# Optimization experiments

Hardware: AMD Instinct MI355X
Metric: run time of the kernel (lower is better)

The kernel has to match this reference:

```python
import jax, jax.numpy as jnp
import numpy as np

TOK_DIM, POS_DIM, HEAD_DIM = 3, 3, 64
D_MODEL, T, B = 128, 4096, 8


def setup_inputs() -> dict:
    key = jax.random.key(0)
    ks = jax.random.split(key, 8)
    s = 0.1
    return {
        "x": jax.random.normal(ks[0], (B, T, TOK_DIM + POS_DIM), jnp.float32),
        "Wq1": jax.random.normal(ks[1], (TOK_DIM, HEAD_DIM), jnp.float32) * s,
        "Wk1": jax.random.normal(ks[2], (TOK_DIM, HEAD_DIM), jnp.float32) * s,
        "Wv1": jax.random.normal(ks[3], (TOK_DIM, HEAD_DIM), jnp.float32) * s,
        "Wq2": jax.random.normal(ks[4], (POS_DIM, HEAD_DIM), jnp.float32) * s,
        "Wk2": jax.random.normal(ks[5], (POS_DIM, HEAD_DIM), jnp.float32) * s,
        "Wv2": jax.random.normal(ks[6], (POS_DIM, HEAD_DIM), jnp.float32) * s,
        "Wout": jax.random.normal(ks[7], (2 * HEAD_DIM, D_MODEL), jnp.float32) * s,
    }


def _attend(q, k, v):
    # q,k,v: [B,T,HEAD_DIM]; causal scaled dot-product attention
    scale = 1.0 / np.sqrt(HEAD_DIM).astype(np.float32)
    scores = jnp.einsum('btd,bsd->bts', q, k) * scale  # [B,T,T]
    t = scores.shape[1]
    causal = jnp.arange(t)[:, None] >= jnp.arange(t)[None, :]
    scores = jnp.where(causal[None], scores, -jnp.inf)
    p = jax.nn.softmax(scores, axis=-1)
    return jnp.einsum('bts,bsd->btd', p, v)


def reference(x, Wq1, Wk1, Wv1, Wq2, Wk2, Wv2, Wout):
    x_tok = x[:, :, :TOK_DIM]
    x_pos = x[:, :, TOK_DIM:]
    out1 = _attend(x_tok @ Wq1, x_tok @ Wk1, x_tok @ Wv1)
    out2 = _attend(x_pos @ Wq2, x_pos @ Wk2, x_pos @ Wv2)
    out = jnp.concatenate([out1, out2], axis=-1)  # [B,T,2*HEAD_DIM]
    return out @ Wout  # [B,T,D_MODEL]
```

## Files before the change

### kernel.cpp

```cpp
#include <hip/hip_runtime.h>
#include <hip/hip_bf16.h>
#include <stdint.h>

#define T_SEQ 4096

typedef float  f32x4   __attribute__((ext_vector_type(4)));
typedef float  f32x16  __attribute__((ext_vector_type(16)));
typedef short  bf16x8  __attribute__((ext_vector_type(8)));
typedef unsigned int u32x2 __attribute__((ext_vector_type(2)));
typedef unsigned int u32x4 __attribute__((ext_vector_type(4)));

typedef const __attribute__((address_space(1))) uint32_t* gptr_t;
typedef __attribute__((address_space(3))) uint32_t* lptr_t;

__device__ __forceinline__ uint32_t f2bf1(float f) {
    uint32_t u = __float_as_uint(f);
    return (u + 0x7fffu + ((u >> 16) & 1u)) >> 16;
}
__device__ __forceinline__ short f2bfs(float f) { return (short)f2bf1(f); }
__device__ __forceinline__ uint32_t cvtpk(float lo, float hi) {
    uint32_t r;
    asm("v_cvt_pk_bf16_f32 %0, %1, %2" : "=v"(r) : "v"(lo), "v"(hi));
    return r;
}

__global__ __launch_bounds__(256) void qk_proj(
    const float* __restrict__ x,
    const float* __restrict__ Wq1, const float* __restrict__ Wk1,
    const float* __restrict__ Wq2, const float* __restrict__ Wk2,
    short* __restrict__ Q, short* __restrict__ K)
{
    int idx = blockIdx.x * 256 + threadIdx.x;
    int d = idx & 63;
    int t = (idx >> 6) & (T_SEQ - 1);
    int b = idx >> 18;
    const float* xp = x + (size_t)(b * T_SEQ + t) * 6;
    float x0 = xp[0], x1 = xp[1], x2 = xp[2];
    float x3 = xp[3], x4 = xp[4], x5 = xp[5];
    const float QS = 0.125f * 1.44269504088896340736f;
    float q1 = (x0 * Wq1[d] + x1 * Wq1[64 + d] + x2 * Wq1[128 + d]) * QS;
    float k1 =  x0 * Wk1[d] + x1 * Wk1[64 + d] + x2 * Wk1[128 + d];
    float q2 = (x3 * Wq2[d] + x4 * Wq2[64 + d] + x5 * Wq2[128 + d]) * QS;
    float k2 =  x3 * Wk2[d] + x4 * Wk2[64 + d] + x5 * Wk2[128 + d];
    size_t base1 = ((size_t)(b * 2 + 0) * T_SEQ + t) * 64 + d;
    size_t base2 = ((size_t)(b * 2 + 1) * T_SEQ + t) * 64 + d;
    Q[base1] = f2bfs(q1);  Q[base2] = f2bfs(q2);
    K[base1] = f2bfs(k1);  K[base2] = f2bfs(k2);
}

__global__ __launch_bounds__(256) void v_proj_t(
    const float* __restrict__ x,
    const float* __restrict__ Wv1, const float* __restrict__ Wv2,
    short* __restrict__ Vt)
{
    int bh = blockIdx.x >> 6;
    int tt = blockIdx.x & 63;
    int head = bh & 1, b = bh >> 1;
    int t  = tt * 64 + (threadIdx.x & 63);
    int dg = threadIdx.x >> 6;
    const float* Wv = head ? Wv2 : Wv1;
    const float* xp = x + (size_t)(b * T_SEQ + t) * 6 + head * 3;
    float x0 = xp[0], x1 = xp[1], x2 = xp[2];
    size_t base = (size_t)bh * 64 * T_SEQ + t;
    #pragma unroll
    for (int k = 0; k < 16; ++k) {
        int d = dg * 16 + k;
        float v = x0 * Wv[d] + x1 * Wv[64 + d] + x2 * Wv[128 + d];
        Vt[base + (size_t)d * T_SEQ] = f2bfs(v);
    }
}

__global__ __launch_bounds__(128, 2) void attn(
    const short* __restrict__ Q, const short* __restrict__ K,
    const short* __restrict__ Vt, float* __restrict__ Hf)
{
    __shared__ __align__(16) char smem[32768];

    int id = blockIdx.x;
    int xcd = id & 7, j = id >> 3;
    int bh = xcd * 2 + (j & 1);
    int i  = j >> 1;
    int tid = threadIdx.x;
    int W = tid >> 6;
    int lane = tid & 63;
    int ql = lane & 31, h = lane >> 5;
    int t0A = 32 * i, t0B = 32 * (127 - i);
    int qA = t0A + ql, qB = t0B + ql;
    int sweep = ((127 - i) >> 1) + 1;

    size_t kvbase = (size_t)bh * (T_SEQ * 64);

    bf16x8 qfA[4], qfB[4];
    #pragma unroll
    for (int ks = 0; ks < 4; ++ks) {
        qfA[ks] = *(const bf16x8*)(Q + kvbase + (size_t)qA * 64 + ks * 16 + h * 8);
        qfB[ks] = *(const bf16x8*)(Q + kvbase + (size_t)qB * 64 + ks * 16 + h * 8);
    }

    int row16 = tid >> 3;
    int scol = ((tid & 7) ^ (row16 & 7)) * 8;
    const short* ksrc = K  + kvbase + (size_t)row16 * 64 + scol;
    const short* vsrc = Vt + kvbase + (size_t)row16 * T_SEQ + scol;

    f32x16 accA0, accA1, accB0, accB1;
    #pragma unroll
    for (int r = 0; r < 16; ++r) { accA0[r]=0.f; accA1[r]=0.f; accB0[r]=0.f; accB1[r]=0.f; }
    float lA = 0.f, lB = 0.f;

#define STAGE(nb, kvv)                                                          \
    _Pragma("unroll")                                                           \
    for (int z = 0; z < 4; ++z) {                                               \
        __builtin_amdgcn_global_load_lds(                                       \
            (gptr_t)(ksrc + (size_t)((kvv) + z * 16) * 64),                     \
            (lptr_t)((nb) + z * 2048 + W * 1024), 16, 0, 0);                    \
        __builtin_amdgcn_global_load_lds(                                       \
            (gptr_t)(vsrc + (size_t)(z * 16) * T_SEQ + (kvv)),                  \
            (lptr_t)((nb) + 8192 + z * 2048 + W * 1024), 16, 0, 0);             \
    }

    STAGE(smem, 0);
    __syncthreads();

    int swz = (ql & 7) << 4;

    for (int c = 0; c < sweep; ++c) {
        const int kv0 = c * 64;
        if (c + 1 < sweep) { char* nb = smem + ((c + 1) & 1) * 16384; STAGE(nb, kv0 + 64); }
        const char* ldsK = smem + (c & 1) * 16384;
        const char* ldsV = ldsK + 8192;

        bool actA = (kv0 + 32 * W <= t0A + 31);
        bool actB = (kv0 + 32 * W <= t0B + 31);

        const char* krow = ldsK + (32 * W + ql) * 128;
        bf16x8 kf0 = *(const bf16x8*)(krow + ((0 * 32 + h * 16) ^ swz));
        bf16x8 kf1 = *(const bf16x8*)(krow + ((1 * 32 + h * 16) ^ swz));
        bf16x8 kf2 = *(const bf16x8*)(krow + ((2 * 32 + h * 16) ^ swz));
        bf16x8 kf3 = *(const bf16x8*)(krow + ((3 * 32 + h * 16) ^ swz));

        bf16x8 pfA0, pfA1, pfB0, pfB1;

#define QK_SM(Sv, qfX, qX, lX, pf0, pf1)                                        \
        {                                                                       \
            f32x16 Sv;                                                          \
            _Pragma("unroll") for (int r = 0; r < 16; ++r) Sv[r] = 0.f;         \
            Sv = __builtin_amdgcn_mfma_f32_32x32x16_bf16(kf0, qfX[0], Sv,0,0,0);\
            Sv = __builtin_amdgcn_mfma_f32_32x32x16_bf16(kf1, qfX[1], Sv,0,0,0);\
            Sv = __builtin_amdgcn_mfma_f32_32x32x16_bf16(kf2, qfX[2], Sv,0,0,0);\
            Sv = __builtin_amdgcn_mfma_f32_32x32x16_bf16(kf3, qfX[3], Sv,0,0,0);\
            bool needmask = (kv0 + 32 * W + 31 > qX - ql);    \
            float pp[16];                                                       \
            _Pragma("unroll") for (int r = 0; r < 16; ++r) {                    \
                float pv = __builtin_amdgcn_exp2f(Sv[r]);                       \
                if (needmask) {                                                 \
                    int kv = kv0 + 32 * W + (r & 3) + 8 * (r >> 2) + 4 * h;     \
                    pv = (kv <= qX) ? pv : 0.f;                                 \
                }                                                               \
                pp[r] = pv;                                                     \
            }                                                                   \
            lX += (((pp[0]+pp[1])+(pp[2]+pp[3])) + ((pp[4]+pp[5])+(pp[6]+pp[7])))\
                + (((pp[8]+pp[9])+(pp[10]+pp[11])) + ((pp[12]+pp[13])+(pp[14]+pp[15])));\
            uint32_t pw[8];                                                     \
            _Pragma("unroll") for (int e = 0; e < 8; ++e)                       \
                pw[e] = cvtpk(pp[2*e], pp[2*e+1]);                              \
            {                                                                   \
                uint32_t a0 = pw[0], b0 = pw[2], a1 = pw[1], b1 = pw[3];        \
                asm("v_permlane32_swap_b32 %0, %1" : "+v"(a0), "+v"(b0));       \
                asm("v_permlane32_swap_b32 %0, %1" : "+v"(a1), "+v"(b1));       \
                u32x4 fr = {a0, a1, b0, b1};                                    \
                pf0 = __builtin_bit_cast(bf16x8, fr);                           \
                uint32_t c0 = pw[4], d0 = pw[6], c1 = pw[5], d1 = pw[7];        \
                asm("v_permlane32_swap_b32 %0, %1" : "+v"(c0), "+v"(d0));       \
                asm("v_permlane32_swap_b32 %0, %1" : "+v"(c1), "+v"(d1));       \
                u32x4 fr1 = {c0, c1, d0, d1};                                   \
                pf1 = __builtin_bit_cast(bf16x8, fr1);                          \
            }                                                                   \
        }

        if (actB) QK_SM(SB, qfB, qB, lB, pfB0, pfB1)
        if (actA) QK_SM(SA, qfA, qA, lA, pfA0, pfA1)

        int cb0 = (2 * W + 0) * 32 + h * 16;
        int cb1 = (2 * W + 1) * 32 + h * 16;
        bf16x8 vf00 = *(const bf16x8*)(ldsV + ql * 128        + (cb0 ^ swz));
        bf16x8 vf01 = *(const bf16x8*)(ldsV + ql * 128        + (cb1 ^ swz));
        bf16x8 vf10 = *(const bf16x8*)(ldsV + (32 + ql) * 128 + (cb0 ^ swz));
        bf16x8 vf11 = *(const bf16x8*)(ldsV + (32 + ql) * 128 + (cb1 ^ swz));

        if (actB) {
            accB0 = __builtin_amdgcn_mfma_f32_32x32x16_bf16(vf00, pfB0, accB0, 0, 0, 0);
            accB0 = __builtin_amdgcn_mfma_f32_32x32x16_bf16(vf01, pfB1, accB0, 0, 0, 0);
            accB1 = __builtin_amdgcn_mfma_f32_32x32x16_bf16(vf10, pfB0, accB1, 0, 0, 0);
            accB1 = __builtin_amdgcn_mfma_f32_32x32x16_bf16(vf11, pfB1, accB1, 0, 0, 0);
        }
        if (actA) {
            accA0 = __builtin_amdgcn_mfma_f32_32x32x16_bf16(vf00, pfA0, accA0, 0, 0, 0);
            accA0 = __builtin_amdgcn_mfma_f32_32x32x16_bf16(vf01, pfA1, accA0, 0, 0, 0);
            accA1 = __builtin_amdgcn_mfma_f32_32x32x16_bf16(vf10, pfA0, accA1, 0, 0, 0);
            accA1 = __builtin_amdgcn_mfma_f32_32x32x16_bf16(vf11, pfA1, accA1, 0, 0, 0);
        }
        __syncthreads();
    }
#undef QK_SM
#undef STAGE

    lA += __shfl_xor(lA, 32);
    lB += __shfl_xor(lB, 32);
    float* cbuf = (float*)smem;
    float* lbuf = cbuf + 4608;
    if (W == 0) {
        float* pb = cbuf + 2304 + lane * 36;
        #pragma unroll
        for (int g2 = 0; g2 < 4; ++g2) {
            *(f32x4*)(pb + g2 * 4)      = f32x4{accB0[g2*4+0], accB0[g2*4+1], accB0[g2*4+2], accB0[g2*4+3]};
            *(f32x4*)(pb + 16 + g2 * 4) = f32x4{accB1[g2*4+0], accB1[g2*4+1], accB1[g2*4+2], accB1[g2*4+3]};
        }
        lbuf[64 + lane] = lB;
    } else {
        float* pb = cbuf + lane * 36;
        #pragma unroll
        for (int g2 = 0; g2 < 4; ++g2) {
            *(f32x4*)(pb + g2 * 4)      = f32x4{accA0[g2*4+0], accA0[g2*4+1], accA0[g2*4+2], accA0[g2*4+3]};
            *(f32x4*)(pb + 16 + g2 * 4) = f32x4{accA1[g2*4+0], accA1[g2*4+1], accA1[g2*4+2], accA1[g2*4+3]};
        }
        lbuf[lane] = lA;
    }
    __syncthreads();
    {
        float* pb = cbuf + W * 2304 + lane * 36;
        float lf = (W ? lB : lA) + lbuf[W * 64 + lane];
        float rl = 1.0f / lf;
        int t0 = W ? t0B : t0A;
        f32x16 a0 = W ? accB0 : accA0;
        f32x16 a1 = W ? accB1 : accA1;
        int head = bh & 1, b = bh >> 1;
        float* hp = Hf + ((size_t)(b * T_SEQ) + t0 + ql) * 128 + head * 64 + 4 * h;
        #pragma unroll
        for (int g2 = 0; g2 < 4; ++g2) {
            f32x4 o0 = *(f32x4*)(pb + g2 * 4);
            f32x4 o1 = *(f32x4*)(pb + 16 + g2 * 4);
            f32x4 s0 = { (a0[g2*4+0]+o0[0])*rl, (a0[g2*4+1]+o0[1])*rl,
                         (a0[g2*4+2]+o0[2])*rl, (a0[g2*4+3]+o0[3])*rl };
            *(f32x4*)(hp + 8 * g2) = s0;
            f32x4 s1 = { (a1[g2*4+0]+o1[0])*rl, (a1[g2*4+1]+o1[1])*rl,
                         (a1[g2*4+2]+o1[2])*rl, (a1[g2*4+3]+o1[3])*rl };
            *(f32x4*)(hp + 32 + 8 * g2) = s1;
        }
    }
}

__global__ __launch_bounds__(256) void prep_wt(
    const float* __restrict__ Wout, short* __restrict__ Wt)
{
    int tid = blockIdx.x * 256 + threadIdx.x;
    int j = tid >> 7, k = tid & 127;
    float v = Wout[k * 128 + j];
    int slot = k >> 3;
    Wt[j * 128 + (((slot ^ (j & 7)) << 3) | (k & 7))] = f2bfs(v);
}

__global__ __launch_bounds__(256) void out_proj(
    const float* Hf, const short* __restrict__ Wt, float* out)
{
    __shared__ __align__(16) char lws[32768];
    int tid = threadIdx.x;
    int w = tid >> 6, lane = tid & 63, c = lane & 15, g = lane >> 4;
    int cs = c & 7;
    #pragma unroll
    for (int z = 0; z < 8; ++z)
        __builtin_amdgcn_global_load_lds((gptr_t)(Wt + z * 2048 + w * 512 + lane * 8),
                                         (lptr_t)(lws + z * 4096 + w * 1024), 16, 0, 0);
    __syncthreads();

    int row0 = blockIdx.x * 64 + w * 16;
    bf16x8 af[4];
    const float* hp = Hf + (size_t)(row0 + c) * 128 + g * 8;
    #pragma unroll
    for (int kc = 0; kc < 4; ++kc) {
        f32x4 x0 = *(const f32x4*)(hp + kc * 32);
        f32x4 x1 = *(const f32x4*)(hp + kc * 32 + 4);
        u32x4 wv = { cvtpk(x0[0], x0[1]), cvtpk(x0[2], x0[3]),
                     cvtpk(x1[0], x1[1]), cvtpk(x1[2], x1[3]) };
        af[kc] = __builtin_bit_cast(bf16x8, wv);
    }
    #pragma unroll
    for (int jt = 0; jt < 8; ++jt) {
        f32x4 accum = {0.f, 0.f, 0.f, 0.f};
        #pragma unroll
        for (int kc = 0; kc < 4; ++kc) {
            int row = jt * 16 + c;
            bf16x8 bfr = *(const bf16x8*)(lws + row * 256 + (((kc * 4 + g) ^ cs) << 4));
            accum = __builtin_amdgcn_mfma_f32_16x16x32_bf16(af[kc], bfr, accum, 0, 0, 0);
        }
        #pragma unroll
        for (int r = 0; r < 4; ++r)
            out[(size_t)(row0 + g * 4 + r) * 128 + jt * 16 + c] = accum[r];
    }
}

extern "C" void kernel_launch(void* const* d_in, const int* in_sizes, int n_in,
                              void* d_out, int out_size, void* d_ws, size_t ws_size,
                              hipStream_t stream)
{
    (void)in_sizes; (void)n_in; (void)out_size; (void)ws_size;
    const float* x    = (const float*)d_in[0];
    const float* Wq1  = (const float*)d_in[1];
    const float* Wk1  = (const float*)d_in[2];
    const float* Wv1  = (const float*)d_in[3];
    const float* Wq2  = (const float*)d_in[4];
    const float* Wk2  = (const float*)d_in[5];
    const float* Wv2  = (const float*)d_in[6];
    const float* Wout = (const float*)d_in[7];
    float* out = (float*)d_out;

    char* ws = (char*)d_ws;
    short* Q  = (short*)(ws);
    short* K  = (short*)(ws + (size_t)8  * 1024 * 1024);
    short* Vt = (short*)(ws + (size_t)16 * 1024 * 1024);
    short* Wt = Q;
    float* Hf = out;

    qk_proj <<<8192, 256, 0, stream>>>(x, Wq1, Wk1, Wq2, Wk2, Q, K);
    v_proj_t<<<1024, 256, 0, stream>>>(x, Wv1, Wv2, Vt);
    attn    <<<1024, 128, 0, stream>>>(Q, K, Vt, Hf);
    prep_wt <<<  64, 256, 0, stream>>>(Wout, Wt);
    out_proj<<< 512, 256, 0, stream>>>(Hf, Wt, out);
}
```

Baseline: 95.79 us.

## Split attention KV sweep across three waves and load V directly from global

Grows the attention block from two to three waves, so each sweep iteration covers 96 KV positions and the number of iterations drops. V fragments are now read straight from global memory into registers instead of being staged through LDS, which shrinks shared memory to 24 KB and allows three blocks per CU. The final cross-wave reduction of partial accumulators and row sums becomes a multi-step LDS exchange. The risks are exposed global-load latency for V, extra work on the tail rows, which are clamped at the sequence end, and higher register pressure under the new launch bounds.

```diff
diff --git a/kernel.cpp b/kernel.cpp
--- a/kernel.cpp
+++ b/kernel.cpp
@@ -70,11 +70,11 @@
     }
 }
 
-__global__ __launch_bounds__(128, 2) void attn(
+__global__ __launch_bounds__(192, 3) void attn(
     const short* __restrict__ Q, const short* __restrict__ K,
     const short* __restrict__ Vt, float* __restrict__ Hf)
 {
-    __shared__ __align__(16) char smem[32768];
+    __shared__ __align__(16) char smem[24576];
 
     int id = blockIdx.x;
     int xcd = id & 7, j = id >> 3;
@@ -86,7 +86,7 @@
     int ql = lane & 31, h = lane >> 5;
     int t0A = 32 * i, t0B = 32 * (127 - i);
     int qA = t0A + ql, qB = t0B + ql;
-    int sweep = ((127 - i) >> 1) + 1;
+    int sweep = (t0B + 31) / 96 + 1;
 
     size_t kvbase = (size_t)bh * (T_SEQ * 64);
 
@@ -97,10 +97,12 @@
         qfB[ks] = *(const bf16x8*)(Q + kvbase + (size_t)qB * 64 + ks * 16 + h * 8);
     }
 
-    int row16 = tid >> 3;
-    int scol = ((tid & 7) ^ (row16 & 7)) * 8;
-    const short* ksrc = K  + kvbase + (size_t)row16 * 64 + scol;
-    const short* vsrc = Vt + kvbase + (size_t)row16 * T_SEQ + scol;
+    int r24 = tid >> 3;
+    int scol = ((tid & 7) ^ (r24 & 7)) * 8;
+    const short* ksrc0 = K + kvbase + scol;
+
+    const short* vrow0 = Vt + kvbase + (size_t)ql * T_SEQ;
+    const short* vrow1 = vrow0 + (size_t)32 * T_SEQ;
 
     f32x16 accA0, accA1, accB0, accB1;
     #pragma unroll
@@ -110,12 +112,11 @@
 #define STAGE(nb, kvv)                                                          \
     _Pragma("unroll")                                                           \
     for (int z = 0; z < 4; ++z) {                                               \
+        int srow = (kvv) + z * 24 + r24;                                        \
+        srow = srow > (T_SEQ - 1) ? (T_SEQ - 1) : srow;                         \
         __builtin_amdgcn_global_load_lds(                                       \
-            (gptr_t)(ksrc + (size_t)((kvv) + z * 16) * 64),                     \
-            (lptr_t)((nb) + z * 2048 + W * 1024), 16, 0, 0);                    \
-        __builtin_amdgcn_global_load_lds(                                       \
-            (gptr_t)(vsrc + (size_t)(z * 16) * T_SEQ + (kvv)),                  \
-            (lptr_t)((nb) + 8192 + z * 2048 + W * 1024), 16, 0, 0);             \
+            (gptr_t)(ksrc0 + (size_t)srow * 64),                                \
+            (lptr_t)((nb) + z * 3072 + W * 1024), 16, 0, 0);                    \
     }
 
     STAGE(smem, 0);
@@ -124,10 +125,17 @@
     int swz = (ql & 7) << 4;
 
     for (int c = 0; c < sweep; ++c) {
-        const int kv0 = c * 64;
-        if (c + 1 < sweep) { char* nb = smem + ((c + 1) & 1) * 16384; STAGE(nb, kv0 + 64); }
-        const char* ldsK = smem + (c & 1) * 16384;
-        const char* ldsV = ldsK + 8192;
+        const int kv0 = 96 * c;
+
+        int kvw = kv0 + 32 * W + 8 * h;
+        int kvc = kvw > (T_SEQ - 24) ? (T_SEQ - 24) : kvw;
+        bf16x8 vf00 = *(const bf16x8*)(vrow0 + kvc);
+        bf16x8 vf01 = *(const bf16x8*)(vrow0 + kvc + 16);
+        bf16x8 vf10 = *(const bf16x8*)(vrow1 + kvc);
+        bf16x8 vf11 = *(const bf16x8*)(vrow1 + kvc + 16);
+
+        if (c + 1 < sweep) { char* nb = smem + ((c + 1) & 1) * 12288; STAGE(nb, kv0 + 96); }
+        const char* ldsK = smem + (c & 1) * 12288;
 
         bool actA = (kv0 + 32 * W <= t0A + 31);
         bool actB = (kv0 + 32 * W <= t0B + 31);
@@ -140,7 +148,7 @@
 
         bf16x8 pfA0, pfA1, pfB0, pfB1;
 
-#define QK_SM(Sv, qfX, qX, lX, pf0, pf1)                                        \
+#define QK_SM(qfX, qX, lX, pf0, pf1)                                            \
         {                                                                       \
             f32x16 Sv;                                                          \
             _Pragma("unroll") for (int r = 0; r < 16; ++r) Sv[r] = 0.f;         \
@@ -148,21 +156,21 @@
             Sv = __builtin_amdgcn_mfma_f32_32x32x16_bf16(kf1, qfX[1], Sv,0,0,0);\
             Sv = __builtin_amdgcn_mfma_f32_32x32x16_bf16(kf2, qfX[2], Sv,0,0,0);\
             Sv = __builtin_amdgcn_mfma_f32_32x32x16_bf16(kf3, qfX[3], Sv,0,0,0);\
-            bool needmask = (kv0 + 32 * W + 31 > qX - ql);    \
-            float pp[16];                                                       \
-            _Pragma("unroll") for (int r = 0; r < 16; ++r) {                    \
-                float pv = __builtin_amdgcn_exp2f(Sv[r]);                       \
+            bool needmask = (kv0 + 32 * W + 31 > (qX) - ql);    \
+            uint32_t pw[8];                                                     \
+            float l0 = 0.f, l1 = 0.f;                                           \
+            _Pragma("unroll") for (int e = 0; e < 8; ++e) {                     \
+                float p0 = __builtin_amdgcn_exp2f(Sv[2 * e]);                   \
+                float p1 = __builtin_amdgcn_exp2f(Sv[2 * e + 1]);               \
                 if (needmask) {                                                 \
-                    int kv = kv0 + 32 * W + (r & 3) + 8 * (r >> 2) + 4 * h;     \
-                    pv = (kv <= qX) ? pv : 0.f;                                 \
+                    int kv = kv0 + 32 * W + 4 * h + 2 * (e & 1) + 8 * (e >> 1); \
+                    p0 = (kv     <= (qX)) ? p0 : 0.f;                           \
+                    p1 = (kv + 1 <= (qX)) ? p1 : 0.f;                           \
                 }                                                               \
-                pp[r] = pv;                                                     \
+                l0 += p0; l1 += p1;                                             \
+                pw[e] = cvtpk(p0, p1);                                          \
             }                                                                   \
-            lX += (((pp[0]+pp[1])+(pp[2]+pp[3])) + ((pp[4]+pp[5])+(pp[6]+pp[7])))\
-                + (((pp[8]+pp[9])+(pp[10]+pp[11])) + ((pp[12]+pp[13])+(pp[14]+pp[15])));\
-            uint32_t pw[8];                                                     \
-            _Pragma("unroll") for (int e = 0; e < 8; ++e)                       \
-                pw[e] = cvtpk(pp[2*e], pp[2*e+1]);                              \
+            lX += l0 + l1;                                                      \
             {                                                                   \
                 uint32_t a0 = pw[0], b0 = pw[2], a1 = pw[1], b1 = pw[3];        \
                 asm("v_permlane32_swap_b32 %0, %1" : "+v"(a0), "+v"(b0));       \
@@ -177,15 +185,8 @@
             }                                                                   \
         }
 
-        if (actB) QK_SM(SB, qfB, qB, lB, pfB0, pfB1)
-        if (actA) QK_SM(SA, qfA, qA, lA, pfA0, pfA1)
-
-        int cb0 = (2 * W + 0) * 32 + h * 16;
-        int cb1 = (2 * W + 1) * 32 + h * 16;
-        bf16x8 vf00 = *(const bf16x8*)(ldsV + ql * 128        + (cb0 ^ swz));
-        bf16x8 vf01 = *(const bf16x8*)(ldsV + ql * 128        + (cb1 ^ swz));
-        bf16x8 vf10 = *(const bf16x8*)(ldsV + (32 + ql) * 128 + (cb0 ^ swz));
-        bf16x8 vf11 = *(const bf16x8*)(ldsV + (32 + ql) * 128 + (cb1 ^ swz));
+        if (actB) QK_SM(qfB, qB, lB, pfB0, pfB1)
+        if (actA) QK_SM(qfA, qA, lA, pfA0, pfA1)
 
         if (actB) {
             accB0 = __builtin_amdgcn_mfma_f32_32x32x16_bf16(vf00, pfB0, accB0, 0, 0, 0);
@@ -206,44 +207,92 @@
 
     lA += __shfl_xor(lA, 32);
     lB += __shfl_xor(lB, 32);
-    float* cbuf = (float*)smem;
-    float* lbuf = cbuf + 4608;
+    float* cb = (float*)smem;
+    float* sA = cb + lane * 33;
+    float* sB = cb + (64 + lane) * 33;
+
+    if (W == 2) {
+        #pragma unroll
+        for (int g = 0; g < 4; ++g) {
+            *(f32x4*)(sA + 4 * g)      = f32x4{accA0[4*g+0], accA0[4*g+1], accA0[4*g+2], accA0[4*g+3]};
+            *(f32x4*)(sA + 16 + 4 * g) = f32x4{accA1[4*g+0], accA1[4*g+1], accA1[4*g+2], accA1[4*g+3]};
+            *(f32x4*)(sB + 4 * g)      = f32x4{accB0[4*g+0], accB0[4*g+1], accB0[4*g+2], accB0[4*g+3]};
+            *(f32x4*)(sB + 16 + 4 * g) = f32x4{accB1[4*g+0], accB1[4*g+1], accB1[4*g+2], accB1[4*g+3]};
+        }
+        sA[32] = lA;  sB[32] = lB;
+    }
+    __syncthreads();
     if (W == 0) {
-        float* pb = cbuf + 2304 + lane * 36;
-        #pragma unroll
-        for (int g2 = 0; g2 < 4; ++g2) {
-            *(f32x4*)(pb + g2 * 4)      = f32x4{accB0[g2*4+0], accB0[g2*4+1], accB0[g2*4+2], accB0[g2*4+3]};
-            *(f32x4*)(pb + 16 + g2 * 4) = f32x4{accB1[g2*4+0], accB1[g2*4+1], accB1[g2*4+2], accB1[g2*4+3]};
-        }
-        lbuf[64 + lane] = lB;
-    } else {
-        float* pb = cbuf + lane * 36;
-        #pragma unroll
-        for (int g2 = 0; g2 < 4; ++g2) {
-            *(f32x4*)(pb + g2 * 4)      = f32x4{accA0[g2*4+0], accA0[g2*4+1], accA0[g2*4+2], accA0[g2*4+3]};
-            *(f32x4*)(pb + 16 + g2 * 4) = f32x4{accA1[g2*4+0], accA1[g2*4+1], accA1[g2*4+2], accA1[g2*4+3]};
-        }
-        lbuf[lane] = lA;
-    }
-    __syncthreads();
-    {
-        float* pb = cbuf + W * 2304 + lane * 36;
-        float lf = (W ? lB : lA) + lbuf[W * 64 + lane];
+        #pragma unroll
+        for (int g = 0; g < 4; ++g) {
+            f32x4 u0 = *(f32x4*)(sA + 4 * g);
+            f32x4 u1 = *(f32x4*)(sA + 16 + 4 * g);
+            accA0[4*g+0] += u0[0]; accA0[4*g+1] += u0[1]; accA0[4*g+2] += u0[2]; accA0[4*g+3] += u0[3];
+            accA1[4*g+0] += u1[0]; accA1[4*g+1] += u1[1]; accA1[4*g+2] += u1[2]; accA1[4*g+3] += u1[3];
+        }
+        lA += sA[32];
+    }
+    if (W == 1) {
+        #pragma unroll
+        for (int g = 0; g < 4; ++g) {
+            f32x4 u0 = *(f32x4*)(sB + 4 * g);
+            f32x4 u1 = *(f32x4*)(sB + 16 + 4 * g);
+            accB0[4*g+0] += u0[0]; accB0[4*g+1] += u0[1]; accB0[4*g+2] += u0[2]; accB0[4*g+3] += u0[3];
+            accB1[4*g+0] += u1[0]; accB1[4*g+1] += u1[1]; accB1[4*g+2] += u1[2]; accB1[4*g+3] += u1[3];
+        }
+        lB += sB[32];
+    }
+    __syncthreads();
+    if (W == 0) {
+        #pragma unroll
+        for (int g = 0; g < 4; ++g) {
+            *(f32x4*)(sB + 4 * g)      = f32x4{accB0[4*g+0], accB0[4*g+1], accB0[4*g+2], accB0[4*g+3]};
+            *(f32x4*)(sB + 16 + 4 * g) = f32x4{accB1[4*g+0], accB1[4*g+1], accB1[4*g+2], accB1[4*g+3]};
+        }
+        sB[32] = lB;
+    }
+    if (W == 1) {
+        #pragma unroll
+        for (int g = 0; g < 4; ++g) {
+            *(f32x4*)(sA + 4 * g)      = f32x4{accA0[4*g+0], accA0[4*g+1], accA0[4*g+2], accA0[4*g+3]};
+            *(f32x4*)(sA + 16 + 4 * g) = f32x4{accA1[4*g+0], accA1[4*g+1], accA1[4*g+2], accA1[4*g+3]};
+        }
+        sA[32] = lA;
+    }
+    __syncthreads();
+    if (W < 2) {
+        f32x16 a0, a1;
+        float lf;
+        if (W == 0) {
+            #pragma unroll
+            for (int g = 0; g < 4; ++g) {
+                f32x4 u0 = *(f32x4*)(sA + 4 * g);
+                f32x4 u1 = *(f32x4*)(sA + 16 + 4 * g);
+                accA0[4*g+0] += u0[0]; accA0[4*g+1] += u0[1]; accA0[4*g+2] += u0[2]; accA0[4*g+3] += u0[3];
+                accA1[4*g+0] += u1[0]; accA1[4*g+1] += u1[1]; accA1[4*g+2] += u1[2]; accA1[4*g+3] += u1[3];
+            }
+            lf = lA + sA[32];
+            a0 = accA0; a1 = accA1;
+        } else {
+            #pragma unroll
+            for (int g = 0; g < 4; ++g) {
+                f32x4 u0 = *(f32x4*)(sB + 4 * g);
+                f32x4 u1 = *(f32x4*)(sB + 16 + 4 * g);
+                accB0[4*g+0] += u0[0]; accB0[4*g+1] += u0[1]; accB0[4*g+2] += u0[2]; accB0[4*g+3] += u0[3];
+                accB1[4*g+0] += u1[0]; accB1[4*g+1] += u1[1]; accB1[4*g+2] += u1[2]; accB1[4*g+3] += u1[3];
+            }
+            lf = lB + sB[32];
+            a0 = accB0; a1 = accB1;
+        }
         float rl = 1.0f / lf;
         int t0 = W ? t0B : t0A;
-        f32x16 a0 = W ? accB0 : accA0;
-        f32x16 a1 = W ? accB1 : accA1;
         int head = bh & 1, b = bh >> 1;
         float* hp = Hf + ((size_t)(b * T_SEQ) + t0 + ql) * 128 + head * 64 + 4 * h;
         #pragma unroll
         for (int g2 = 0; g2 < 4; ++g2) {
-            f32x4 o0 = *(f32x4*)(pb + g2 * 4);
-            f32x4 o1 = *(f32x4*)(pb + 16 + g2 * 4);
-            f32x4 s0 = { (a0[g2*4+0]+o0[0])*rl, (a0[g2*4+1]+o0[1])*rl,
-                         (a0[g2*4+2]+o0[2])*rl, (a0[g2*4+3]+o0[3])*rl };
+            f32x4 s0 = { a0[g2*4+0]*rl, a0[g2*4+1]*rl, a0[g2*4+2]*rl, a0[g2*4+3]*rl };
             *(f32x4*)(hp + 8 * g2) = s0;
-            f32x4 s1 = { (a1[g2*4+0]+o1[0])*rl, (a1[g2*4+1]+o1[1])*rl,
-                         (a1[g2*4+2]+o1[2])*rl, (a1[g2*4+3]+o1[3])*rl };
+            f32x4 s1 = { a1[g2*4+0]*rl, a1[g2*4+1]*rl, a1[g2*4+2]*rl, a1[g2*4+3]*rl };
             *(f32x4*)(hp + 32 + 8 * g2) = s1;
         }
     }
@@ -322,7 +371,7 @@
 
     qk_proj <<<8192, 256, 0, stream>>>(x, Wq1, Wk1, Wq2, Wk2, Q, K);
     v_proj_t<<<1024, 256, 0, stream>>>(x, Wv1, Wv2, Vt);
-    attn    <<<1024, 128, 0, stream>>>(Q, K, Vt, Hf);
+    attn    <<<1024, 192, 0, stream>>>(Q, K, Vt, Hf);
     prep_wt <<<  64, 256, 0, stream>>>(Wout, Wt);
     out_proj<<< 512, 256, 0, stream>>>(Hf, Wt, out);
 }
```

Result: slower. 155.5 us (+62.3%).

## Load V directly to registers and per-wave K staging without block barriers

Applied to the files above, without the earlier changes.

Restructures the attention main loop so each wave stages only its own 32 K rows into LDS and loads its V fragments straight from global memory into registers. The loop is unrolled by two with register double-buffering and two-deep prefetch, and per-iteration __syncthreads is replaced by s_waitcnt vmcnt. It also raises MFMA priority with s_setprio, interleaves exp with bf16 packing, and shrinks LDS use. The aim is to remove block-level barriers and LDS traffic for V. The risks are that V global loads are less coalesced, and that relying on vmcnt ordering with no barrier is fragile.

```diff
diff --git a/kernel.cpp b/kernel.cpp
--- a/kernel.cpp
+++ b/kernel.cpp
@@ -7,7 +7,6 @@
 typedef float  f32x4   __attribute__((ext_vector_type(4)));
 typedef float  f32x16  __attribute__((ext_vector_type(16)));
 typedef short  bf16x8  __attribute__((ext_vector_type(8)));
-typedef unsigned int u32x2 __attribute__((ext_vector_type(2)));
 typedef unsigned int u32x4 __attribute__((ext_vector_type(4)));
 
 typedef const __attribute__((address_space(1))) uint32_t* gptr_t;
@@ -74,7 +73,7 @@
     const short* __restrict__ Q, const short* __restrict__ K,
     const short* __restrict__ Vt, float* __restrict__ Hf)
 {
-    __shared__ __align__(16) char smem[32768];
+    __shared__ __align__(16) char smem[19456];
 
     int id = blockIdx.x;
     int xcd = id & 7, j = id >> 3;
@@ -97,50 +96,43 @@
         qfB[ks] = *(const bf16x8*)(Q + kvbase + (size_t)qB * 64 + ks * 16 + h * 8);
     }
 
-    int row16 = tid >> 3;
-    int scol = ((tid & 7) ^ (row16 & 7)) * 8;
-    const short* ksrc = K  + kvbase + (size_t)row16 * 64 + scol;
-    const short* vsrc = Vt + kvbase + (size_t)row16 * T_SEQ + scol;
+    int r8 = lane >> 3;
+    int scol = ((lane & 7) ^ r8) * 8;
+    const short* ksrc0 = K + kvbase + scol;
+
+    const short* vrow0 = Vt + kvbase + (size_t)ql * T_SEQ;
+    const short* vrow1 = vrow0 + (size_t)32 * T_SEQ;
 
     f32x16 accA0, accA1, accB0, accB1;
     #pragma unroll
     for (int r = 0; r < 16; ++r) { accA0[r]=0.f; accA1[r]=0.f; accB0[r]=0.f; accB1[r]=0.f; }
     float lA = 0.f, lB = 0.f;
-
-#define STAGE(nb, kvv)                                                          \
-    _Pragma("unroll")                                                           \
-    for (int z = 0; z < 4; ++z) {                                               \
-        __builtin_amdgcn_global_load_lds(                                       \
-            (gptr_t)(ksrc + (size_t)((kvv) + z * 16) * 64),                     \
-            (lptr_t)((nb) + z * 2048 + W * 1024), 16, 0, 0);                    \
-        __builtin_amdgcn_global_load_lds(                                       \
-            (gptr_t)(vsrc + (size_t)(z * 16) * T_SEQ + (kvv)),                  \
-            (lptr_t)((nb) + 8192 + z * 2048 + W * 1024), 16, 0, 0);             \
-    }
-
-    STAGE(smem, 0);
-    __syncthreads();
-
     int swz = (ql & 7) << 4;
 
-    for (int c = 0; c < sweep; ++c) {
-        const int kv0 = c * 64;
-        if (c + 1 < sweep) { char* nb = smem + ((c + 1) & 1) * 16384; STAGE(nb, kv0 + 64); }
-        const char* ldsK = smem + (c & 1) * 16384;
-        const char* ldsV = ldsK + 8192;
-
-        bool actA = (kv0 + 32 * W <= t0A + 31);
-        bool actB = (kv0 + 32 * W <= t0B + 31);
-
-        const char* krow = ldsK + (32 * W + ql) * 128;
-        bf16x8 kf0 = *(const bf16x8*)(krow + ((0 * 32 + h * 16) ^ swz));
-        bf16x8 kf1 = *(const bf16x8*)(krow + ((1 * 32 + h * 16) ^ swz));
-        bf16x8 kf2 = *(const bf16x8*)(krow + ((2 * 32 + h * 16) ^ swz));
-        bf16x8 kf3 = *(const bf16x8*)(krow + ((3 * 32 + h * 16) ^ swz));
-
-        bf16x8 pfA0, pfA1, pfB0, pfB1;
-
-#define QK_SM(Sv, qfX, qX, lX, pf0, pf1)                                        \
+#define STAGEK(bsel, kvv)                                                       \
+    {                                                                           \
+        char* kb = smem + (bsel) * 8192 + W * 4096;                             \
+        _Pragma("unroll")                                                       \
+        for (int z = 0; z < 4; ++z) {                                           \
+            int srow = (kvv) + 32 * W + z * 8 + r8;                             \
+            srow = srow > (T_SEQ - 1) ? (T_SEQ - 1) : srow;                     \
+            __builtin_amdgcn_global_load_lds(                                   \
+                (gptr_t)(ksrc0 + (size_t)srow * 64),                            \
+                (lptr_t)(kb + z * 1024), 16, 0, 0);                             \
+        }                                                                       \
+    }
+
+#define VISSUE(v0, v1, v2, v3, kvv)                                             \
+    {                                                                           \
+        int kvw = (kvv) + 32 * W + 8 * h;                                       \
+        int kvc = kvw > (T_SEQ - 24) ? (T_SEQ - 24) : kvw;                      \
+        v0 = *(const bf16x8*)(vrow0 + kvc);                                     \
+        v1 = *(const bf16x8*)(vrow0 + kvc + 16);                                \
+        v2 = *(const bf16x8*)(vrow1 + kvc);                                     \
+        v3 = *(const bf16x8*)(vrow1 + kvc + 16);                                \
+    }
+
+#define QK_SM(qfX, qX, lX, pf0, pf1)                                            \
         {                                                                       \
             f32x16 Sv;                                                          \
             _Pragma("unroll") for (int r = 0; r < 16; ++r) Sv[r] = 0.f;         \
@@ -148,21 +140,21 @@
             Sv = __builtin_amdgcn_mfma_f32_32x32x16_bf16(kf1, qfX[1], Sv,0,0,0);\
             Sv = __builtin_amdgcn_mfma_f32_32x32x16_bf16(kf2, qfX[2], Sv,0,0,0);\
             Sv = __builtin_amdgcn_mfma_f32_32x32x16_bf16(kf3, qfX[3], Sv,0,0,0);\
-            bool needmask = (kv0 + 32 * W + 31 > qX - ql);    \
-            float pp[16];                                                       \
-            _Pragma("unroll") for (int r = 0; r < 16; ++r) {                    \
-                float pv = __builtin_amdgcn_exp2f(Sv[r]);                       \
+            bool needmask = (kv0 + 32 * W + 31 > (qX) - ql);    \
+            uint32_t pw[8];                                                     \
+            float l0 = 0.f, l1 = 0.f;                                           \
+            _Pragma("unroll") for (int e = 0; e < 8; ++e) {                     \
+                float p0 = __builtin_amdgcn_exp2f(Sv[2 * e]);                   \
+                float p1 = __builtin_amdgcn_exp2f(Sv[2 * e + 1]);               \
                 if (needmask) {                                                 \
-                    int kv = kv0 + 32 * W + (r & 3) + 8 * (r >> 2) + 4 * h;     \
-                    pv = (kv <= qX) ? pv : 0.f;                                 \
+                    int kv = kv0 + 32 * W + 4 * h + 2 * (e & 1) + 8 * (e >> 1); \
+                    p0 = (kv     <= (qX)) ? p0 : 0.f;                           \
+                    p1 = (kv + 1 <= (qX)) ? p1 : 0.f;                           \
                 }                                                               \
-                pp[r] = pv;                                                     \
+                l0 += p0; l1 += p1;                                             \
+                pw[e] = cvtpk(p0, p1);                                          \
             }                                                                   \
-            lX += (((pp[0]+pp[1])+(pp[2]+pp[3])) + ((pp[4]+pp[5])+(pp[6]+pp[7])))\
-                + (((pp[8]+pp[9])+(pp[10]+pp[11])) + ((pp[12]+pp[13])+(pp[14]+pp[15])));\
-            uint32_t pw[8];                                                     \
-            _Pragma("unroll") for (int e = 0; e < 8; ++e)                       \
-                pw[e] = cvtpk(pp[2*e], pp[2*e+1]);                              \
+            lX += l0 + l1;                                                      \
             {                                                                   \
                 uint32_t a0 = pw[0], b0 = pw[2], a1 = pw[1], b1 = pw[3];        \
                 asm("v_permlane32_swap_b32 %0, %1" : "+v"(a0), "+v"(b0));       \
@@ -177,33 +169,57 @@
             }                                                                   \
         }
 
-        if (actB) QK_SM(SB, qfB, qB, lB, pfB0, pfB1)
-        if (actA) QK_SM(SA, qfA, qA, lA, pfA0, pfA1)
-
-        int cb0 = (2 * W + 0) * 32 + h * 16;
-        int cb1 = (2 * W + 1) * 32 + h * 16;
-        bf16x8 vf00 = *(const bf16x8*)(ldsV + ql * 128        + (cb0 ^ swz));
-        bf16x8 vf01 = *(const bf16x8*)(ldsV + ql * 128        + (cb1 ^ swz));
-        bf16x8 vf10 = *(const bf16x8*)(ldsV + (32 + ql) * 128 + (cb0 ^ swz));
-        bf16x8 vf11 = *(const bf16x8*)(ldsV + (32 + ql) * 128 + (cb1 ^ swz));
-
-        if (actB) {
-            accB0 = __builtin_amdgcn_mfma_f32_32x32x16_bf16(vf00, pfB0, accB0, 0, 0, 0);
-            accB0 = __builtin_amdgcn_mfma_f32_32x32x16_bf16(vf01, pfB1, accB0, 0, 0, 0);
-            accB1 = __builtin_amdgcn_mfma_f32_32x32x16_bf16(vf10, pfB0, accB1, 0, 0, 0);
-            accB1 = __builtin_amdgcn_mfma_f32_32x32x16_bf16(vf11, pfB1, accB1, 0, 0, 0);
-        }
-        if (actA) {
-            accA0 = __builtin_amdgcn_mfma_f32_32x32x16_bf16(vf00, pfA0, accA0, 0, 0, 0);
-            accA0 = __builtin_amdgcn_mfma_f32_32x32x16_bf16(vf01, pfA1, accA0, 0, 0, 0);
-            accA1 = __builtin_amdgcn_mfma_f32_32x32x16_bf16(vf10, pfA0, accA1, 0, 0, 0);
-            accA1 = __builtin_amdgcn_mfma_f32_32x32x16_bf16(vf11, pfA1, accA1, 0, 0, 0);
-        }
-        __syncthreads();
-    }
+#define BODY(cc, v0, v1, v2, v3)                                                \
+    {                                                                           \
+        const int kv0 = (cc) * 64;                                              \
+        asm volatile("s_waitcnt vmcnt(8)" ::: "memory");                        \
+        const char* krow = smem + ((cc) & 1) * 8192 + W * 4096 + ql * 128;      \
+        bf16x8 kf0 = *(const bf16x8*)(krow + ((0 * 32 + h * 16) ^ swz));        \
+        bf16x8 kf1 = *(const bf16x8*)(krow + ((1 * 32 + h * 16) ^ swz));        \
+        bf16x8 kf2 = *(const bf16x8*)(krow + ((2 * 32 + h * 16) ^ swz));        \
+        bf16x8 kf3 = *(const bf16x8*)(krow + ((3 * 32 + h * 16) ^ swz));        \
+        bool actA = (kv0 + 32 * W <= t0A + 31);                                 \
+        bool actB = (kv0 + 32 * W <= t0B + 31);                                 \
+        bf16x8 pfA0, pfA1, pfB0, pfB1;                                          \
+        __builtin_amdgcn_s_setprio(1);                                          \
+        if (actB) QK_SM(qfB, qB, lB, pfB0, pfB1)                                \
+        if (actA) QK_SM(qfA, qA, lA, pfA0, pfA1)                                \
+        if (actB) {                                                             \
+            accB0 = __builtin_amdgcn_mfma_f32_32x32x16_bf16(v0, pfB0, accB0, 0, 0, 0); \
+            accB0 = __builtin_amdgcn_mfma_f32_32x32x16_bf16(v1, pfB1, accB0, 0, 0, 0); \
+            accB1 = __builtin_amdgcn_mfma_f32_32x32x16_bf16(v2, pfB0, accB1, 0, 0, 0); \
+            accB1 = __builtin_amdgcn_mfma_f32_32x32x16_bf16(v3, pfB1, accB1, 0, 0, 0); \
+        }                                                                       \
+        if (actA) {                                                             \
+            accA0 = __builtin_amdgcn_mfma_f32_32x32x16_bf16(v0, pfA0, accA0, 0, 0, 0); \
+            accA0 = __builtin_amdgcn_mfma_f32_32x32x16_bf16(v1, pfA1, accA0, 0, 0, 0); \
+            accA1 = __builtin_amdgcn_mfma_f32_32x32x16_bf16(v2, pfA0, accA1, 0, 0, 0); \
+            accA1 = __builtin_amdgcn_mfma_f32_32x32x16_bf16(v3, pfA1, accA1, 0, 0, 0); \
+        }                                                                       \
+        __builtin_amdgcn_s_setprio(0);                                          \
+        VISSUE(v0, v1, v2, v3, kv0 + 128);                                      \
+        STAGEK((cc) & 1, kv0 + 128);                                            \
+    }
+
+    bf16x8 vfA0, vfA1, vfA2, vfA3, vfB0, vfB1, vfB2, vfB3;
+    VISSUE(vfA0, vfA1, vfA2, vfA3, 0);
+    STAGEK(0, 0);
+    VISSUE(vfB0, vfB1, vfB2, vfB3, 64);
+    STAGEK(1, 64);
+
+    int c = 0;
+    for (;;) {
+        BODY(c, vfA0, vfA1, vfA2, vfA3);
+        if (++c >= sweep) break;
+        BODY(c, vfB0, vfB1, vfB2, vfB3);
+        if (++c >= sweep) break;
+    }
+#undef BODY
 #undef QK_SM
-#undef STAGE
-
+#undef VISSUE
+#undef STAGEK
+
+    __syncthreads();
     lA += __shfl_xor(lA, 32);
     lB += __shfl_xor(lB, 32);
     float* cbuf = (float*)smem;
```

Result: slower. 105.7 us (+10.4%).
